# Kernel tuning notes

Measured on AMD Instinct MI355X. Metric: run time of the kernel, lower is better.

The kernel has to match this reference:

```python
import jax, jax.numpy as jnp
import numpy as np

N = 50000      # nodes
E = 800000     # edges
G = 512        # graphs in the batch
CAT = 32       # node category count
D = 128        # node_emb_dim == gnn_hidden_dim
H = 8          # gat heads
C = 16         # out channels per head (D // H)
EF = 8         # raw edge feature dim
EE = 64        # edge_emb_dim
L = 4          # gnn layers
NCLS = 10
NEG = jnp.float32(-1e9)
BN_EPS = 1e-5


def setup_inputs() -> dict:
    ks = jax.random.split(jax.random.key(0), 24)
    g = lambda k, shape, scale: jax.random.normal(ks[k], shape, jnp.float32) * scale
    return {
        "x_nodes": jax.random.randint(ks[0], (N,), 0, CAT),
        "edge_src": jax.random.randint(ks[1], (E,), 0, N),
        "edge_dst": jax.random.randint(ks[2], (E,), 0, N),
        "edge_attr": g(3, (E, EF), 1.0),
        "batch": jnp.sort(jax.random.randint(ks[4], (N,), 0, G)),
        "node_emb": g(5, (CAT, D), 1.0),
        "edge_W": g(6, (EF, EE), EF ** -0.5),
        "edge_b": jnp.zeros((EE,), jnp.float32),
        "Wl": g(7, (L, D, H * C), D ** -0.5),
        "bl": g(8, (L, H * C), 0.02),
        "Wr": g(9, (L, D, H * C), D ** -0.5),
        "br": g(10, (L, H * C), 0.02),
        "We": g(11, (L, EE, H * C), EE ** -0.5),
        "att": g(12, (L, H, C), C ** -0.5),
        "gbias": g(13, (L, H * C), 0.02),
        "bn_gamma": 1.0 + g(14, (L, H * C), 0.05),
        "bn_beta": g(15, (L, H * C), 0.02),
        "head_W": g(16, (D, NCLS), D ** -0.5),
        "head_b": jnp.zeros((NCLS,), jnp.float32),
    }


def reference(x_nodes, edge_src, edge_dst, edge_attr, batch, node_emb,
              edge_W, edge_b, Wl, bl, Wr, br, We, att, gbias,
              bn_gamma, bn_beta, head_W, head_b):
    x = node_emb[x_nodes]                                    # [N, D] node encoder
    eattr = edge_attr @ edge_W + edge_b                      # [E, EE] edge encoder

    # GATv2Conv add_self_loops: remove existing self loops (masking keeps static
    # shapes), then append one self loop per node with edge_attr = per-node mean
    # of incoming edge attrs (PyG fill_value='mean').
    mask = edge_src != edge_dst                              # [E]
    w = mask.astype(jnp.float32)[:, None]
    cnt = jnp.clip(jax.ops.segment_sum(w, edge_dst, N), 1.0)
    loop_attr = jax.ops.segment_sum(eattr * w, edge_dst, N) / cnt  # [N, EE]
    ea = jnp.concatenate([eattr, loop_attr], axis=0)         # [E+N, EE]
    idx = jnp.arange(N)
    s = jnp.concatenate([edge_src, idx])                     # [E+N]
    d = jnp.concatenate([edge_dst, idx])
    mall = jnp.concatenate([mask, jnp.ones((N,), bool)])

    for i in range(L):
        xl = (x @ Wl[i] + bl[i]).reshape(N, H, C)            # source transform
        xr = (x @ Wr[i] + br[i]).reshape(N, H, C)            # target transform
        ep = (ea @ We[i]).reshape(-1, H, C)                  # edge transform
        z = jax.nn.leaky_relu(xl[s] + xr[d] + ep, 0.2)       # [E+N, H, C]
        logits = jnp.einsum('ehc,hc->eh', z, att[i])         # [E+N, H]
        logits = jnp.where(mall[:, None], logits, NEG)
        # segment softmax over target node d (each node has a self loop -> nonempty)
        m = jax.ops.segment_max(logits, d, num_segments=N)   # [N, H]
        p = jnp.where(mall[:, None], jnp.exp(logits - m[d]), 0.0)
        alpha = p / jax.ops.segment_sum(p, d, N)[d]          # [E+N, H]
        h = jax.ops.segment_sum(alpha[..., None] * xl[s], d, N)  # [N, H, C]
        h = h.reshape(N, H * C) + gbias[i]
        # BatchNorm1d in eval mode with running stats (mean=0, var=1)
        h = bn_gamma[i] * h * (1.0 + BN_EPS) ** -0.5 + bn_beta[i]
        x = jax.nn.elu(h)                                    # dropout inactive (eval)

    # global mean pool over graphs
    gsum = jax.ops.segment_sum(x, batch, G)                  # [G, D]
    gcnt = jnp.clip(jax.ops.segment_sum(jnp.ones((N, 1), jnp.float32), batch, G), 1.0)
    return (gsum / gcnt) @ head_W + head_b                   # [G, NCLS]
```

## Files before the change

### kernel.cpp

```cpp
#include <hip/hip_runtime.h>
#include <hip/hip_fp16.h>
#include <math.h>

static constexpr int N  = 50000;
static constexpr int E  = 800000;
static constexpr int G  = 512;
static constexpr int D  = 128;
static constexpr int EF = 8;
static constexpr int EE = 64;
static constexpr int L  = 4;
static constexpr int NC = 10;

typedef _Float16 half8 __attribute__((ext_vector_type(8)));
typedef _Float16 h2v  __attribute__((ext_vector_type(2)));
typedef float f2v __attribute__((ext_vector_type(2)));
typedef float f32x4 __attribute__((ext_vector_type(4)));

union H4 { float4 f4; h2v h[4]; };

#if __has_builtin(__builtin_amdgcn_fdot2)
#define FDOT2(a, b, c) __builtin_amdgcn_fdot2((a), (b), (c), false)
#else
#define FDOT2(a, b, c) ((float)(a)[0]*(float)(b)[0] + (float)(a)[1]*(float)(b)[1] + (c))
#endif

__device__ __forceinline__ h2v pkrtz(float a, float b) {
    return (h2v)__builtin_amdgcn_cvt_pkrtz(a, b);
}
__device__ __forceinline__ h2v hmax2(h2v a, h2v b) {
#if __has_builtin(__builtin_elementwise_max)
    return __builtin_elementwise_max(a, b);
#else
    h2v r; r[0] = a[0] > b[0] ? a[0] : b[0]; r[1] = a[1] > b[1] ? a[1] : b[1]; return r;
#endif
}
__device__ __forceinline__ h2v hfma2(h2v a, h2v b, h2v c) {
#if __has_builtin(__builtin_elementwise_fma)
    return __builtin_elementwise_fma(a, b, c);
#else
    return a * b + c;
#endif
}
__device__ __forceinline__ float red8(float v) {
#if __has_builtin(__builtin_amdgcn_update_dpp)
    v += __builtin_bit_cast(float, __builtin_amdgcn_update_dpp(
            0, __builtin_bit_cast(int, v), 0xB1, 0xF, 0xF, true));
    v += __builtin_bit_cast(float, __builtin_amdgcn_update_dpp(
            0, __builtin_bit_cast(int, v), 0x4E, 0xF, 0xF, true));
    v += __builtin_bit_cast(float, __builtin_amdgcn_update_dpp(
            0, __builtin_bit_cast(int, v), 0x141, 0xF, 0xF, true));
#else
    v += __shfl_xor(v, 1); v += __shfl_xor(v, 2); v += __shfl_xor(v, 4);
#endif
    return v;
}

#define LOG2E 1.44269504088896340736f

static constexpr size_t pad64(size_t w){ return (w + 63) & ~size_t(63); }
static constexpr size_t O_CNT     = 0;
static constexpr size_t O_CURSOR  = O_CNT + pad64(N);
static constexpr size_t ZERO_END  = O_CURSOR + pad64(N);
static constexpr size_t O_CSROFF  = ZERO_END;
static constexpr size_t O_BSUM    = O_CSROFF + pad64(N+1);
static constexpr size_t O_CSRSRC  = O_BSUM + 64;
static constexpr size_t O_CSREA   = O_CSRSRC + pad64(E);
static constexpr size_t O_MH      = O_CSREA + pad64((size_t)E*4);
static constexpr size_t O_CFOLD   = O_MH + pad64((size_t)L*512);
static constexpr size_t O_LOOPM   = O_CFOLD + pad64(L*D);
static constexpr size_t O_SELFF   = O_LOOPM + pad64((size_t)N*4);
static constexpr size_t O_WFRAG   = O_SELFF + pad64(N);
static constexpr size_t O_XH      = O_WFRAG + pad64((size_t)L*16384);
static constexpr size_t O_XLH     = O_XH  + pad64((size_t)N*64);
static constexpr size_t O_XRH     = O_XLH + pad64((size_t)N*64);

static constexpr int PB_EMB  = (N * D) / 256;
static constexpr int PB_ZERO = ((int)ZERO_END + 255) / 256;
static constexpr int PB_WCVT = (L * 32768) / 256;
static constexpr int PB_FOLD = L;
static constexpr int PB_TOTAL = PB_EMB + PB_ZERO + PB_WCVT + PB_FOLD;

__global__ __launch_bounds__(256) void prep_kernel(
        const int* __restrict__ xn, const float* __restrict__ emb, __half* __restrict__ xh,
        float* __restrict__ zbase,
        const float* __restrict__ Wl, const float* __restrict__ Wr, _Float16* __restrict__ wfrag,
        const float* __restrict__ edge_W, const float* __restrict__ edge_b,
        const float* __restrict__ We, _Float16* __restrict__ Mh, float* __restrict__ cfold) {
    int bid = blockIdx.x, t = threadIdx.x;
    if (bid < PB_EMB) {
        int i = bid * 256 + t;
        int n = i >> 7, c = i & 127;
        xh[i] = __float2half_rn(emb[xn[n] * D + c]);
    } else if (bid < PB_EMB + PB_ZERO) {
        int i = (bid - PB_EMB) * 256 + t;
        if (i < (int)ZERO_END) zbase[i] = 0.0f;
    } else if (bid < PB_EMB + PB_ZERO + PB_WCVT) {
        int i = (bid - PB_EMB - PB_ZERO) * 256 + t;
        int j    = i & 7;
        int lane = (i >> 3) & 63;
        int nt   = (i >> 9) & 15;
        int kt   = (i >> 13) & 3;
        int l    = i >> 15;
        int k = kt * 32 + (lane >> 4) * 8 + j;
        int n = nt * 16 + (lane & 15);
        float v = (n < 128) ? Wl[((size_t)l * D + k) * D + n]
                            : Wr[((size_t)l * D + k) * D + (n - 128)];
        wfrag[i] = (_Float16)v;
    } else {
        int l = bid - PB_EMB - PB_ZERO - PB_WCVT;
        if (t >= 128) return;
        const float* Wel = We + (size_t)l * EE * D;
        for (int j = 0; j < EF; ++j) {
            float s = 0.f;
            for (int k = 0; k < EE; ++k) s += edge_W[j * EE + k] * Wel[k * D + t];
            Mh[((size_t)l * D + t) * 8 + j] = (_Float16)s;
        }
        float s = 0.f;
        for (int k = 0; k < EE; ++k) s += edge_b[k] * Wel[k * D + t];
        cfold[l * D + t] = s;
    }
}

__global__ void edge_cnt_kernel(const int* __restrict__ src, const int* __restrict__ dst,
                                int* __restrict__ cnt) {
    int e = blockIdx.x * blockDim.x + threadIdx.x;
    if (e >= E) return;
    if (src[e] != dst[e]) atomicAdd(&cnt[dst[e]], 1);
}

__global__ void scan1_kernel(const int* __restrict__ cnt, int* __restrict__ out ,
                             int* __restrict__ bsum) {
    __shared__ int lds[256];
    int b = blockIdx.x, t = threadIdx.x;
    int base = b * 1024 + t * 4;
    int v[4]; int s = 0;
    #pragma unroll
    for (int k = 0; k < 4; ++k) { int idx = base + k; v[k] = (idx < N) ? cnt[idx] : 0; s += v[k]; }
    lds[t] = s; __syncthreads();
    for (int off = 1; off < 256; off <<= 1) {
        int add = (t >= off) ? lds[t - off] : 0;
        __syncthreads();
        lds[t] += add;
        __syncthreads();
    }
    int run = (t > 0) ? lds[t - 1] : 0;
    #pragma unroll
    for (int k = 0; k < 4; ++k) { run += v[k]; int idx = base + k; if (idx < N) out[idx] = run; }
    if (t == 255) bsum[b] = lds[255];
}

__global__ void scan3_kernel(int* __restrict__ csr_off, const int* __restrict__ bsum) {
    int i = blockIdx.x * blockDim.x + threadIdx.x;
    if (i == 0) csr_off[0] = 0;
    if (i >= N) return;
    int b = i >> 10;
    int add = 0;
    for (int k = 0; k < b; ++k) add += bsum[k];
    csr_off[1 + i] += add;
}

__global__ void csr_fill_kernel(const int* __restrict__ src, const int* __restrict__ dst,
                                const float* __restrict__ eattr,
                                const int* __restrict__ csr_off, int* __restrict__ cursor,
                                int* __restrict__ csr_src, __half* __restrict__ csr_ea) {
    int e = blockIdx.x * blockDim.x + threadIdx.x;
    if (e >= E) return;
    int s = src[e], d = dst[e];
    if (s == d) return;
    int pos = csr_off[d] + atomicAdd(&cursor[d], 1);
    csr_src[pos] = s << 8;
    const float4* p = reinterpret_cast<const float4*>(eattr + (size_t)e * 8);
    float4 a = p[0], b = p[1];
    __half2 h[4];
    h[0] = __floats2half2_rn(a.x, a.y); h[1] = __floats2half2_rn(a.z, a.w);
    h[2] = __floats2half2_rn(b.x, b.y); h[3] = __floats2half2_rn(b.z, b.w);
    *reinterpret_cast<float4*>(csr_ea + (size_t)pos * 8) = *reinterpret_cast<const float4*>(h);
}

__global__ void loopmean_kernel(const int* __restrict__ csr_off, const __half* __restrict__ csr_ea,
                                __half* __restrict__ loopm, float* __restrict__ selff) {
    int i = blockIdx.x * blockDim.x + threadIdx.x;
    int n = i >> 3, j = i & 7;
    if (n >= N) return;
    int beg = csr_off[n], end = csr_off[n + 1];
    float s = 0.f;
    for (int idx = beg; idx < end; ++idx) s += __half2float(csr_ea[(size_t)idx * 8 + j]);
    int c = end - beg;
    loopm[(size_t)n * 8 + j] = __float2half_rn(s / (float)(c > 1 ? c : 1));
    if (j == 0) selff[n] = (c > 0) ? 1.0f : 0.0f;
}

__global__ __launch_bounds__(256) void transform_kernel(
        const __half* __restrict__ xh, const _Float16* __restrict__ wfrag,
        const float* __restrict__ bl, const float* __restrict__ br,
        __half* __restrict__ xl_h, __half* __restrict__ xr_h) {
    int w = threadIdx.x >> 6, lane = threadIdx.x & 63;
    int quad = lane >> 4, r16 = lane & 15;
    int m0 = blockIdx.x * 16;
    const _Float16* xrow = reinterpret_cast<const _Float16*>(xh) + (size_t)(m0 + r16) * D + quad * 8;
    half8 a[4];
    #pragma unroll
    for (int kt = 0; kt < 4; ++kt) a[kt] = *reinterpret_cast<const half8*>(xrow + kt * 32);
    f32x4 acc[4];
    #pragma unroll
    for (int nt = 0; nt < 4; ++nt) { f32x4 z = {0.f, 0.f, 0.f, 0.f}; acc[nt] = z; }
    #pragma unroll
    for (int nt = 0; nt < 4; ++nt) {
        int ntile = w * 4 + nt;
        #pragma unroll
        for (int kt = 0; kt < 4; ++kt) {
            half8 b = *reinterpret_cast<const half8*>(
                wfrag + ((size_t)(kt * 16 + ntile) * 64 + lane) * 8);
            acc[nt] = __builtin_amdgcn_mfma_f32_16x16x32_f16(a[kt], b, acc[nt], 0, 0, 0);
        }
    }
    #pragma unroll
    for (int nt = 0; nt < 4; ++nt) {
        int n = (w * 4 + nt) * 16 + r16;
        float bias = (n < 128) ? bl[n] : br[n - 128];
        #pragma unroll
        for (int r = 0; r < 4; ++r) {
            int node = m0 + quad * 4 + r;
            float v = acc[nt][r] + bias;
            if (n < 128) xl_h[(size_t)node * D + n] = __float2half_rn(v);
            else         xr_h[(size_t)node * D + (n - 128)] = __float2half_rn(v);
        }
    }
}

__global__ __launch_bounds__(64) void aggregate_kernel(
        const __half* __restrict__ xl_h, const __half* __restrict__ xr_h,
        const __half* __restrict__ loopm, const float* __restrict__ selff,
        const int* __restrict__ csr_off, const int* __restrict__ csr_src,
        const __half* __restrict__ csr_ea,
        const _Float16* __restrict__ Mh, const float* __restrict__ cfold,
        const float* __restrict__ att, const float* __restrict__ gbias,
        const float* __restrict__ bn_gamma, const float* __restrict__ bn_beta,
        __half* __restrict__ xout) {
    int n = blockIdx.x;
    int t = threadIdx.x;
    int c0 = t * 2;
    const char* xlb = reinterpret_cast<const char*>(xl_h);
    int lb = t << 2;
    h2v attp = pkrtz(att[c0] * LOG2E, att[c0 + 1] * LOG2E);
    H4 m0u, m1u;
    m0u.f4 = *reinterpret_cast<const float4*>(Mh + (size_t)c0 * 8);
    m1u.f4 = *reinterpret_cast<const float4*>(Mh + (size_t)(c0 + 1) * 8);
    float cf0 = cfold[c0], cf1 = cfold[c0 + 1];
    h2v xrp = *reinterpret_cast<const h2v*>(xr_h + (size_t)n * D + c0);
    h2v xlp = *reinterpret_cast<const h2v*>(xl_h + (size_t)n * D + c0);
    const h2v c02 = {(_Float16)0.2f, (_Float16)0.2f};

    H4 lau;
    lau.f4 = *reinterpret_cast<const float4*>(loopm + (size_t)n * 8);
    float sf = selff[n];
    float ep0 = cf0 * sf, ep1 = cf1 * sf;
    #pragma unroll
    for (int k = 0; k < 4; ++k) { ep0 = FDOT2(lau.h[k], m0u.h[k], ep0); ep1 = FDOT2(lau.h[k], m1u.h[k], ep1); }
    {
        f2v xlf = __builtin_convertvector(xlp, f2v);
        f2v xrf = __builtin_convertvector(xrp, f2v);
        float z0 = xlf[0] + xrf[0] + ep0; z0 = fmaxf(z0, 0.2f * z0);
        float z1 = xlf[1] + xrf[1] + ep1; z1 = fmaxf(z1, 0.2f * z1);
        ep0 = FDOT2(pkrtz(z0, z1), attp, 0.0f);
    }
    float m = red8(ep0);
    float denom = 1.0f;
    h2v acc = xlp;

    int beg = csr_off[n], end = csr_off[n + 1];
    for (int base = beg; base < end; base += 64) {
        int cnt = end - base; if (cnt > 64) cnt = 64;
        int sreg = (t < cnt) ? csr_src[base + t] : 0;
        int i = 0;
        for (; i + 4 <= cnt; i += 4) {
            int o0 = __shfl(sreg, i),     o1 = __shfl(sreg, i + 1);
            int o2 = __shfl(sreg, i + 2), o3 = __shfl(sreg, i + 3);
            h2v g0 = *reinterpret_cast<const h2v*>(xlb + o0 + lb);
            h2v g1 = *reinterpret_cast<const h2v*>(xlb + o1 + lb);
            h2v g2 = *reinterpret_cast<const h2v*>(xlb + o2 + lb);
            h2v g3 = *reinterpret_cast<const h2v*>(xlb + o3 + lb);
            H4 e0u, e1u, e2u, e3u;
            e0u.f4 = *reinterpret_cast<const float4*>(csr_ea + (size_t)(base + i) * 8);
            e1u.f4 = *reinterpret_cast<const float4*>(csr_ea + (size_t)(base + i) * 8 + 8);
            e2u.f4 = *reinterpret_cast<const float4*>(csr_ea + (size_t)(base + i) * 8 + 16);
            e3u.f4 = *reinterpret_cast<const float4*>(csr_ea + (size_t)(base + i) * 8 + 24);
            float p00 = cf0, p01 = cf1, p10 = cf0, p11 = cf1;
            float p20 = cf0, p21 = cf1, p30 = cf0, p31 = cf1;
            #pragma unroll
            for (int k = 0; k < 4; ++k) {
                p00 = FDOT2(e0u.h[k], m0u.h[k], p00); p01 = FDOT2(e0u.h[k], m1u.h[k], p01);
                p10 = FDOT2(e1u.h[k], m0u.h[k], p10); p11 = FDOT2(e1u.h[k], m1u.h[k], p11);
                p20 = FDOT2(e2u.h[k], m0u.h[k], p20); p21 = FDOT2(e2u.h[k], m1u.h[k], p21);
                p30 = FDOT2(e3u.h[k], m0u.h[k], p30); p31 = FDOT2(e3u.h[k], m1u.h[k], p31);
            }
            h2v z0 = g0 + xrp + pkrtz(p00, p01);
            h2v z1 = g1 + xrp + pkrtz(p10, p11);
            h2v z2 = g2 + xrp + pkrtz(p20, p21);
            h2v z3 = g3 + xrp + pkrtz(p30, p31);
            z0 = hmax2(z0, z0 * c02); z1 = hmax2(z1, z1 * c02);
            z2 = hmax2(z2, z2 * c02); z3 = hmax2(z3, z3 * c02);
            float l0 = red8(FDOT2(z0, attp, 0.0f));
            float l1 = red8(FDOT2(z1, attp, 0.0f));
            float l2 = red8(FDOT2(z2, attp, 0.0f));
            float l3 = red8(FDOT2(z3, attp, 0.0f));
            float gm = fmaxf(fmaxf(l0, l1), fmaxf(l2, l3));
            float nm = fmaxf(m, gm);
            float wo = __builtin_amdgcn_exp2f(m - nm);
            float w0 = __builtin_amdgcn_exp2f(l0 - nm);
            float w1 = __builtin_amdgcn_exp2f(l1 - nm);
            float w2 = __builtin_amdgcn_exp2f(l2 - nm);
            float w3 = __builtin_amdgcn_exp2f(l3 - nm);
            denom = denom * wo + (w0 + w1) + (w2 + w3);
            acc = acc * pkrtz(wo, wo);
            acc = hfma2(pkrtz(w0, w0), g0, acc);
            acc = hfma2(pkrtz(w1, w1), g1, acc);
            acc = hfma2(pkrtz(w2, w2), g2, acc);
            acc = hfma2(pkrtz(w3, w3), g3, acc);
            m = nm;
        }
        for (; i < cnt; ++i) {
            int o0 = __shfl(sreg, i);
            h2v g0 = *reinterpret_cast<const h2v*>(xlb + o0 + lb);
            H4 e0u;
            e0u.f4 = *reinterpret_cast<const float4*>(csr_ea + (size_t)(base + i) * 8);
            float p00 = cf0, p01 = cf1;
            #pragma unroll
            for (int k = 0; k < 4; ++k) { p00 = FDOT2(e0u.h[k], m0u.h[k], p00); p01 = FDOT2(e0u.h[k], m1u.h[k], p01); }
            h2v z0 = g0 + xrp + pkrtz(p00, p01);
            z0 = hmax2(z0, z0 * c02);
            float l0 = red8(FDOT2(z0, attp, 0.0f));
            float nm = fmaxf(m, l0);
            float wo = __builtin_amdgcn_exp2f(m - nm);
            float w0 = __builtin_amdgcn_exp2f(l0 - nm);
            denom = denom * wo + w0;
            acc = acc * pkrtz(wo, wo);
            acc = hfma2(pkrtz(w0, w0), g0, acc);
            m = nm;
        }
    }
    f2v accf = __builtin_convertvector(acc, f2v);
    float inv = 1.0f / denom;
    float h0 = accf[0] * inv + gbias[c0];
    float h1 = accf[1] * inv + gbias[c0 + 1];
    h0 = bn_gamma[c0] * h0 * 0.999995000037499813f + bn_beta[c0];
    h1 = bn_gamma[c0 + 1] * h1 * 0.999995000037499813f + bn_beta[c0 + 1];
    h0 = h0 > 0.f ? h0 : (__expf(h0) - 1.0f);
    h1 = h1 > 0.f ? h1 : (__expf(h1) - 1.0f);
    *reinterpret_cast<__half2*>(xout + (size_t)n * D + c0) = __floats2half2_rn(h0, h1);
}

__device__ __forceinline__ int lower_bound_dev(const int* a, int n, int v) {
    int lo = 0, hi = n;
    while (lo < hi) { int mid = (lo + hi) >> 1; if (a[mid] < v) lo = mid + 1; else hi = mid; }
    return lo;
}

__global__ __launch_bounds__(128) void headpool_kernel(
        const __half* __restrict__ xh, const int* __restrict__ batch,
        const float* __restrict__ hW, const float* __restrict__ hb,
        float* __restrict__ out) {
    __shared__ float lds[128];
    int g = blockIdx.x, t = threadIdx.x;
    int lo = lower_bound_dev(batch, N, g);
    int hi = lower_bound_dev(batch, N, g + 1);
    float s = 0.f;
    #pragma unroll 4
    for (int i = lo; i < hi; ++i) s += __half2float(xh[(size_t)i * D + t]);
    int c = hi - lo;
    lds[t] = s / (float)(c > 1 ? c : 1);
    __syncthreads();
    if (t < NC) {
        float p = hb[t];
        #pragma unroll 8
        for (int cc = 0; cc < D; ++cc) p += lds[cc] * hW[cc * NC + t];
        out[g * NC + t] = p;
    }
}

extern "C" void kernel_launch(void* const* d_in, const int* in_sizes, int n_in,
                              void* d_out, int out_size, void* d_ws, size_t ws_size,
                              hipStream_t stream) {
    const int*   x_nodes   = (const int*)  d_in[0];
    const int*   edge_src  = (const int*)  d_in[1];
    const int*   edge_dst  = (const int*)  d_in[2];
    const float* edge_attr = (const float*)d_in[3];
    const int*   batch     = (const int*)  d_in[4];
    const float* node_emb  = (const float*)d_in[5];
    const float* edge_W    = (const float*)d_in[6];
    const float* edge_b    = (const float*)d_in[7];
    const float* Wl        = (const float*)d_in[8];
    const float* bl        = (const float*)d_in[9];
    const float* Wr        = (const float*)d_in[10];
    const float* br        = (const float*)d_in[11];
    const float* We        = (const float*)d_in[12];
    const float* att       = (const float*)d_in[13];
    const float* gbias     = (const float*)d_in[14];
    const float* bn_gamma  = (const float*)d_in[15];
    const float* bn_beta   = (const float*)d_in[16];
    const float* head_W    = (const float*)d_in[17];
    const float* head_b    = (const float*)d_in[18];
    float* out = (float*)d_out;

    float* ws = (float*)d_ws;
    int*    cnt      = (int*)(ws + O_CNT);
    int*    cursor   = (int*)(ws + O_CURSOR);
    int*    csr_off  = (int*)(ws + O_CSROFF);
    int*    bsum     = (int*)(ws + O_BSUM);
    int*    csr_src  = (int*)(ws + O_CSRSRC);
    __half* csr_ea   = (__half*)(ws + O_CSREA);
    _Float16* Mh     = (_Float16*)(ws + O_MH);
    float*  cfold    = ws + O_CFOLD;
    __half* loopm    = (__half*)(ws + O_LOOPM);
    float*  selff    = ws + O_SELFF;
    _Float16* wfrag  = (_Float16*)(ws + O_WFRAG);
    __half* xh   = (__half*)(ws + O_XH);
    __half* xl_h = (__half*)(ws + O_XLH);
    __half* xr_h = (__half*)(ws + O_XRH);

    prep_kernel<<<PB_TOTAL, 256, 0, stream>>>(x_nodes, node_emb, xh, ws,
                                              Wl, Wr, wfrag, edge_W, edge_b, We, Mh, cfold);
    edge_cnt_kernel<<<(E + 255) / 256, 256, 0, stream>>>(edge_src, edge_dst, cnt);
    {
        int nb = (N + 1023) / 1024;
        scan1_kernel<<<nb, 256, 0, stream>>>(cnt, csr_off + 1, bsum);
        scan3_kernel<<<(N + 255) / 256, 256, 0, stream>>>(csr_off, bsum);
    }
    csr_fill_kernel<<<(E + 255) / 256, 256, 0, stream>>>(edge_src, edge_dst, edge_attr,
                                                         csr_off, cursor, csr_src, csr_ea);
    loopmean_kernel<<<(N * 8 + 255) / 256, 256, 0, stream>>>(csr_off, csr_ea, loopm, selff);
    for (int l = 0; l < L; ++l) {
        transform_kernel<<<N / 16, 256, 0, stream>>>(
            xh, wfrag + (size_t)l * 32768, bl + l * D, br + l * D, xl_h, xr_h);
        aggregate_kernel<<<N, 64, 0, stream>>>(
            xl_h, xr_h, loopm, selff, csr_off, csr_src, csr_ea,
            Mh + (size_t)l * D * 8, cfold + l * D, att + l * D, gbias + l * D,
            bn_gamma + l * D, bn_beta + l * D, xh);
    }
    headpool_kernel<<<G, 128, 0, stream>>>(xh, batch, head_W, head_b, out);

    (void)in_sizes; (void)n_in; (void)out_size; (void)ws_size;
}
```

Measured before the change: 532.9 us.

## Store edge ids in CSR and gather edge attrs; pack four nodes per aggregate block

The CSR fill no longer writes a permuted copy of the fp16 edge attributes. The edge attributes are converted to fp16 once, in original edge order, inside the prep kernel, and the CSR stores (src offset, edge id) pairs. Aggregation and loop-mean then gather attributes indirectly by edge id, which turns the contiguous reads into random 16-byte gathers in every layer. Separately, the aggregate kernel now runs four nodes per 256-thread block instead of one node per 64-thread block, cutting the block count. The intent is to make the fill step cheaper and improve scheduling, at the cost of less coalesced attribute reads during aggregation.

Result: slower. 567.4 us (+6.5%).

```diff
diff --git a/kernel.cpp b/kernel.cpp
--- a/kernel.cpp
+++ b/kernel.cpp
@@ -63,9 +63,9 @@
 static constexpr size_t ZERO_END  = O_CURSOR + pad64(N);
 static constexpr size_t O_CSROFF  = ZERO_END;
 static constexpr size_t O_BSUM    = O_CSROFF + pad64(N+1);
-static constexpr size_t O_CSRSRC  = O_BSUM + 64;
-static constexpr size_t O_CSREA   = O_CSRSRC + pad64(E);
-static constexpr size_t O_MH      = O_CSREA + pad64((size_t)E*4);
+static constexpr size_t O_CSRMETA = O_BSUM + 64;
+static constexpr size_t O_EAH     = O_CSRMETA + pad64((size_t)E*2);
+static constexpr size_t O_MH      = O_EAH + pad64((size_t)E*4);
 static constexpr size_t O_CFOLD   = O_MH + pad64((size_t)L*512);
 static constexpr size_t O_LOOPM   = O_CFOLD + pad64(L*D);
 static constexpr size_t O_SELFF   = O_LOOPM + pad64((size_t)N*4);
@@ -76,13 +76,15 @@
 
 static constexpr int PB_EMB  = (N * D) / 256;
 static constexpr int PB_ZERO = ((int)ZERO_END + 255) / 256;
+static constexpr int PB_EAH  = E / 256;
 static constexpr int PB_WCVT = (L * 32768) / 256;
 static constexpr int PB_FOLD = L;
-static constexpr int PB_TOTAL = PB_EMB + PB_ZERO + PB_WCVT + PB_FOLD;
+static constexpr int PB_TOTAL = PB_EMB + PB_ZERO + PB_EAH + PB_WCVT + PB_FOLD;
 
 __global__ __launch_bounds__(256) void prep_kernel(
         const int* __restrict__ xn, const float* __restrict__ emb, __half* __restrict__ xh,
         float* __restrict__ zbase,
+        const float* __restrict__ eattr, __half* __restrict__ eah,
         const float* __restrict__ Wl, const float* __restrict__ Wr, _Float16* __restrict__ wfrag,
         const float* __restrict__ edge_W, const float* __restrict__ edge_b,
         const float* __restrict__ We, _Float16* __restrict__ Mh, float* __restrict__ cfold) {
@@ -94,8 +96,16 @@
     } else if (bid < PB_EMB + PB_ZERO) {
         int i = (bid - PB_EMB) * 256 + t;
         if (i < (int)ZERO_END) zbase[i] = 0.0f;
-    } else if (bid < PB_EMB + PB_ZERO + PB_WCVT) {
-        int i = (bid - PB_EMB - PB_ZERO) * 256 + t;
+    } else if (bid < PB_EMB + PB_ZERO + PB_EAH) {
+        int e = (bid - PB_EMB - PB_ZERO) * 256 + t;
+        const float4* p = reinterpret_cast<const float4*>(eattr + (size_t)e * 8);
+        float4 a = p[0], b = p[1];
+        __half2 h[4];
+        h[0] = __floats2half2_rn(a.x, a.y); h[1] = __floats2half2_rn(a.z, a.w);
+        h[2] = __floats2half2_rn(b.x, b.y); h[3] = __floats2half2_rn(b.z, b.w);
+        *reinterpret_cast<float4*>(eah + (size_t)e * 8) = *reinterpret_cast<const float4*>(h);
+    } else if (bid < PB_EMB + PB_ZERO + PB_EAH + PB_WCVT) {
+        int i = (bid - PB_EMB - PB_ZERO - PB_EAH) * 256 + t;
         int j    = i & 7;
         int lane = (i >> 3) & 63;
         int nt   = (i >> 9) & 15;
@@ -107,7 +117,7 @@
                             : Wr[((size_t)l * D + k) * D + (n - 128)];
         wfrag[i] = (_Float16)v;
     } else {
-        int l = bid - PB_EMB - PB_ZERO - PB_WCVT;
+        int l = bid - PB_EMB - PB_ZERO - PB_EAH - PB_WCVT;
         if (t >= 128) return;
         const float* Wel = We + (size_t)l * EE * D;
         for (int j = 0; j < EF; ++j) {
@@ -160,31 +170,28 @@
 }
 
 __global__ void csr_fill_kernel(const int* __restrict__ src, const int* __restrict__ dst,
-                                const float* __restrict__ eattr,
                                 const int* __restrict__ csr_off, int* __restrict__ cursor,
-                                int* __restrict__ csr_src, __half* __restrict__ csr_ea) {
+                                int2* __restrict__ csr_meta) {
     int e = blockIdx.x * blockDim.x + threadIdx.x;
     if (e >= E) return;
     int s = src[e], d = dst[e];
     if (s == d) return;
     int pos = csr_off[d] + atomicAdd(&cursor[d], 1);
-    csr_src[pos] = s << 8;
-    const float4* p = reinterpret_cast<const float4*>(eattr + (size_t)e * 8);
-    float4 a = p[0], b = p[1];
-    __half2 h[4];
-    h[0] = __floats2half2_rn(a.x, a.y); h[1] = __floats2half2_rn(a.z, a.w);
-    h[2] = __floats2half2_rn(b.x, b.y); h[3] = __floats2half2_rn(b.z, b.w);
-    *reinterpret_cast<float4*>(csr_ea + (size_t)pos * 8) = *reinterpret_cast<const float4*>(h);
-}
-
-__global__ void loopmean_kernel(const int* __restrict__ csr_off, const __half* __restrict__ csr_ea,
+    csr_meta[pos] = make_int2(s << 8, e);
+}
+
+__global__ void loopmean_kernel(const int* __restrict__ csr_off, const int2* __restrict__ csr_meta,
+                                const __half* __restrict__ eah,
                                 __half* __restrict__ loopm, float* __restrict__ selff) {
     int i = blockIdx.x * blockDim.x + threadIdx.x;
     int n = i >> 3, j = i & 7;
     if (n >= N) return;
     int beg = csr_off[n], end = csr_off[n + 1];
     float s = 0.f;
-    for (int idx = beg; idx < end; ++idx) s += __half2float(csr_ea[(size_t)idx * 8 + j]);
+    for (int idx = beg; idx < end; ++idx) {
+        int eid = csr_meta[idx].y;
+        s += __half2float(eah[(size_t)eid * 8 + j]);
+    }
     int c = end - beg;
     loopm[(size_t)n * 8 + j] = __float2half_rn(s / (float)(c > 1 ? c : 1));
     if (j == 0) selff[n] = (c > 0) ? 1.0f : 0.0f;
@@ -228,19 +235,20 @@
     }
 }
 
-__global__ __launch_bounds__(64) void aggregate_kernel(
+__global__ __launch_bounds__(256) void aggregate_kernel(
         const __half* __restrict__ xl_h, const __half* __restrict__ xr_h,
         const __half* __restrict__ loopm, const float* __restrict__ selff,
-        const int* __restrict__ csr_off, const int* __restrict__ csr_src,
-        const __half* __restrict__ csr_ea,
+        const int* __restrict__ csr_off, const int2* __restrict__ csr_meta,
+        const __half* __restrict__ eah,
         const _Float16* __restrict__ Mh, const float* __restrict__ cfold,
         const float* __restrict__ att, const float* __restrict__ gbias,
         const float* __restrict__ bn_gamma, const float* __restrict__ bn_beta,
         __half* __restrict__ xout) {
-    int n = blockIdx.x;
-    int t = threadIdx.x;
+    int n = blockIdx.x * 4 + (threadIdx.x >> 6);
+    int t = threadIdx.x & 63;
     int c0 = t * 2;
     const char* xlb = reinterpret_cast<const char*>(xl_h);
+    const char* eab = reinterpret_cast<const char*>(eah);
     int lb = t << 2;
     h2v attp = pkrtz(att[c0] * LOG2E, att[c0 + 1] * LOG2E);
     H4 m0u, m1u;
@@ -271,20 +279,22 @@
     int beg = csr_off[n], end = csr_off[n + 1];
     for (int base = beg; base < end; base += 64) {
         int cnt = end - base; if (cnt > 64) cnt = 64;
-        int sreg = (t < cnt) ? csr_src[base + t] : 0;
+        int2 sreg = (t < cnt) ? csr_meta[base + t] : make_int2(0, 0);
         int i = 0;
         for (; i + 4 <= cnt; i += 4) {
-            int o0 = __shfl(sreg, i),     o1 = __shfl(sreg, i + 1);
-            int o2 = __shfl(sreg, i + 2), o3 = __shfl(sreg, i + 3);
+            int o0 = __shfl(sreg.x, i),     o1 = __shfl(sreg.x, i + 1);
+            int o2 = __shfl(sreg.x, i + 2), o3 = __shfl(sreg.x, i + 3);
+            int e0 = __shfl(sreg.y, i),     e1 = __shfl(sreg.y, i + 1);
+            int e2 = __shfl(sreg.y, i + 2), e3 = __shfl(sreg.y, i + 3);
             h2v g0 = *reinterpret_cast<const h2v*>(xlb + o0 + lb);
             h2v g1 = *reinterpret_cast<const h2v*>(xlb + o1 + lb);
             h2v g2 = *reinterpret_cast<const h2v*>(xlb + o2 + lb);
             h2v g3 = *reinterpret_cast<const h2v*>(xlb + o3 + lb);
             H4 e0u, e1u, e2u, e3u;
-            e0u.f4 = *reinterpret_cast<const float4*>(csr_ea + (size_t)(base + i) * 8);
-            e1u.f4 = *reinterpret_cast<const float4*>(csr_ea + (size_t)(base + i) * 8 + 8);
-            e2u.f4 = *reinterpret_cast<const float4*>(csr_ea + (size_t)(base + i) * 8 + 16);
-            e3u.f4 = *reinterpret_cast<const float4*>(csr_ea + (size_t)(base + i) * 8 + 24);
+            e0u.f4 = *reinterpret_cast<const float4*>(eab + ((size_t)e0 << 4));
+            e1u.f4 = *reinterpret_cast<const float4*>(eab + ((size_t)e1 << 4));
+            e2u.f4 = *reinterpret_cast<const float4*>(eab + ((size_t)e2 << 4));
+            e3u.f4 = *reinterpret_cast<const float4*>(eab + ((size_t)e3 << 4));
             float p00 = cf0, p01 = cf1, p10 = cf0, p11 = cf1;
             float p20 = cf0, p21 = cf1, p30 = cf0, p31 = cf1;
             #pragma unroll
@@ -320,10 +330,11 @@
             m = nm;
         }
         for (; i < cnt; ++i) {
-            int o0 = __shfl(sreg, i);
+            int o0 = __shfl(sreg.x, i);
+            int e0 = __shfl(sreg.y, i);
             h2v g0 = *reinterpret_cast<const h2v*>(xlb + o0 + lb);
             H4 e0u;
-            e0u.f4 = *reinterpret_cast<const float4*>(csr_ea + (size_t)(base + i) * 8);
+            e0u.f4 = *reinterpret_cast<const float4*>(eab + ((size_t)e0 << 4));
             float p00 = cf0, p01 = cf1;
             #pragma unroll
             for (int k = 0; k < 4; ++k) { p00 = FDOT2(e0u.h[k], m0u.h[k], p00); p01 = FDOT2(e0u.h[k], m1u.h[k], p01); }
@@ -407,8 +418,8 @@
     int*    cursor   = (int*)(ws + O_CURSOR);
     int*    csr_off  = (int*)(ws + O_CSROFF);
     int*    bsum     = (int*)(ws + O_BSUM);
-    int*    csr_src  = (int*)(ws + O_CSRSRC);
-    __half* csr_ea   = (__half*)(ws + O_CSREA);
+    int2*   csr_meta = (int2*)(ws + O_CSRMETA);
+    __half* eah      = (__half*)(ws + O_EAH);
     _Float16* Mh     = (_Float16*)(ws + O_MH);
     float*  cfold    = ws + O_CFOLD;
     __half* loopm    = (__half*)(ws + O_LOOPM);
@@ -418,7 +429,7 @@
     __half* xl_h = (__half*)(ws + O_XLH);
     __half* xr_h = (__half*)(ws + O_XRH);
 
-    prep_kernel<<<PB_TOTAL, 256, 0, stream>>>(x_nodes, node_emb, xh, ws,
+    prep_kernel<<<PB_TOTAL, 256, 0, stream>>>(x_nodes, node_emb, xh, ws, edge_attr, eah,
                                               Wl, Wr, wfrag, edge_W, edge_b, We, Mh, cfold);
     edge_cnt_kernel<<<(E + 255) / 256, 256, 0, stream>>>(edge_src, edge_dst, cnt);
     {
@@ -426,14 +437,15 @@
         scan1_kernel<<<nb, 256, 0, stream>>>(cnt, csr_off + 1, bsum);
         scan3_kernel<<<(N + 255) / 256, 256, 0, stream>>>(csr_off, bsum);
     }
-    csr_fill_kernel<<<(E + 255) / 256, 256, 0, stream>>>(edge_src, edge_dst, edge_attr,
-                                                         csr_off, cursor, csr_src, csr_ea);
-    loopmean_kernel<<<(N * 8 + 255) / 256, 256, 0, stream>>>(csr_off, csr_ea, loopm, selff);
+    csr_fill_kernel<<<(E + 255) / 256, 256, 0, stream>>>(edge_src, edge_dst,
+                                                         csr_off, cursor, csr_meta);
+    loopmean_kernel<<<(N * 8 + 255) / 256, 256, 0, stream>>>(csr_off, csr_meta, eah,
+                                                             loopm, selff);
     for (int l = 0; l < L; ++l) {
         transform_kernel<<<N / 16, 256, 0, stream>>>(
             xh, wfrag + (size_t)l * 32768, bl + l * D, br + l * D, xl_h, xr_h);
-        aggregate_kernel<<<N, 64, 0, stream>>>(
-            xl_h, xr_h, loopm, selff, csr_off, csr_src, csr_ea,
+        aggregate_kernel<<<N / 4, 256, 0, stream>>>(
+            xl_h, xr_h, loopm, selff, csr_off, csr_meta, eah,
             Mh + (size_t)l * D * 8, cfold + l * D, att + l * D, gbias + l * D,
             bn_gamma + l * D, bn_beta + l * D, xh);
     }
```
